# Optimization experiments

Hardware: AMD Instinct MI355X
Metric: run time of the kernel (lower is better)

## Reference

```python
import jax, jax.numpy as jnp
import numpy as np
from jax import lax

START_TAG = 29
STOP_TAG = 30
PAD_TAG = 31
NEG_INF = -10000.0


def setup_inputs() -> dict:
    key = jax.random.key(0)
    k_feat, k_trans, k_len = jax.random.split(key, 3)
    S, B, T = 1024, 1024, 32
    feats = jax.random.normal(k_feat, (S, B, T), dtype=jnp.float32)
    # left-aligned padding mask with random lengths in [S//2, S]
    lengths = jax.random.randint(k_len, (B,), S // 2, S + 1)
    mask = (jnp.arange(S)[:, None] < lengths[None, :]).astype(jnp.float32)  # [S,B]
    transitions = jax.random.normal(k_trans, (T, T), dtype=jnp.float32)
    # replicate the constraint initialization from __init__
    transitions = transitions.at[START_TAG, :].set(NEG_INF)
    transitions = transitions.at[:, STOP_TAG].set(NEG_INF)
    transitions = transitions.at[:, PAD_TAG].set(NEG_INF)
    transitions = transitions.at[PAD_TAG, :].set(NEG_INF)
    transitions = transitions.at[PAD_TAG, STOP_TAG].set(0.0)
    transitions = transitions.at[PAD_TAG, PAD_TAG].set(0.0)
    # zero emissions at padded steps, as _get_lstm_features does (feats * mask)
    feats = feats * mask[:, :, None]
    return {"feats": feats, "mask": mask, "transitions": transitions}


def reference(feats, mask, transitions):
    """CRF forward algorithm (log partition) + Viterbi max-score scan.

    feats: [S, B, T] emission scores, mask: [S, B] float, transitions: [T, T]
    (transitions[i, j] = score of transitioning from tag j to tag i).
    Returns (logZ [B], best_score [B], pointers [S, B, T] int32).
    """
    S, B, T = feats.shape

    alpha0 = jnp.full((B, T), NEG_INF, dtype=feats.dtype).at[:, START_TAG].set(0.0)

    def fwd_step(alpha, xs):
        feat, m = xs  # feat [B,T], m [B]
        # alpha_t[b, i, j] = alpha[b, j] + transitions[i, j] + feat[b, i]
        alpha_t = alpha[:, None, :] + transitions[None, :, :] + feat[:, :, None]
        new = jax.nn.logsumexp(alpha_t, axis=-1)  # [B,T]
        m = m[:, None]
        return new * m + alpha * (1.0 - m), None

    alpha, _ = lax.scan(fwd_step, alpha0, (feats, mask))
    logZ = jax.nn.logsumexp(alpha + transitions[STOP_TAG][None, :], axis=-1)  # [B]

    def vit_step(scores, xs):
        feat, m = xs
        scores_t = scores[:, None, :] + transitions[None, :, :]  # [B,T,T]
        best = jnp.max(scores_t, axis=-1)                        # [B,T]
        ptr = jnp.argmax(scores_t, axis=-1).astype(jnp.int32)    # [B,T]
        scores_t = best + feat
        m = m[:, None]
        return scores_t * m + scores * (1.0 - m), ptr

    scores0 = jnp.full((B, T), NEG_INF, dtype=feats.dtype).at[:, START_TAG].set(0.0)
    scores, pointers = lax.scan(vit_step, scores0, (feats, mask))
    scores = scores + transitions[STOP_TAG][None, :]
    best_score = jnp.max(scores, axis=-1)  # [B]
    return logZ, best_score, pointers
```

## Files before the change

### kernel.cpp

```cpp
#include <hip/hip_runtime.h>


#define SS 1024
#define BB 1024
#define TT 32
#define POFF (2 * BB)

__global__ __launch_bounds__(64) void crf_split_kernel(
    const float* __restrict__ feats,
    const float* __restrict__ mask,
    const float* __restrict__ trans,
    float* __restrict__ out) {

  const int b    = blockIdx.x;
  const int lane = threadIdx.x;
  const int g    = lane >> 5;
  const int i    = lane & 31;
  const int j0   = g << 4;

  __shared__ __align__(16) float row[TT];

  const float t_stop = trans[30 * TT + i];

  float f[4], mk[4];
#pragma unroll
  for (int u = 0; u < 4; ++u) {
    f[u]  = feats[(u * BB + b) * TT + i];
    mk[u] = mask[u * BB + b];
  }

  if (blockIdx.y == 0) {
    float er[16];
#pragma unroll
    for (int k = 0; k < 16; ++k)
      er[k] = __expf(trans[i * TT + j0 + k]);

    float alpha = (i == 29) ? 0.0f : -10000.0f;
    float M = 0.0f;

#pragma unroll 1
    for (int s = 0; s < SS; s += 4) {
      float nf[4], nm[4];
#pragma unroll
      for (int u = 0; u < 4; ++u) {
        int su = (s + 4 + u < SS) ? (s + 4 + u) : 0;
        nf[u] = feats[(su * BB + b) * TT + i];
        nm[u] = mask[su * BB + b];
      }
#pragma unroll
      for (int u = 0; u < 4; ++u) {
        if (mk[u] == 0.0f) goto fwd_done;
        float p = __expf(alpha - M);
        row[i] = p;
        __builtin_amdgcn_wave_barrier();
        float4 p0 = *(const float4*)&row[j0];
        float4 p1 = *(const float4*)&row[j0 + 4];
        float4 p2 = *(const float4*)&row[j0 + 8];
        float4 p3 = *(const float4*)&row[j0 + 12];
        __builtin_amdgcn_wave_barrier();
        float a0 = er[0] * p0.x, a1 = er[1] * p0.y;
        float a2 = er[2] * p0.z, a3 = er[3] * p0.w;
        a0 = fmaf(er[4],  p1.x, a0); a1 = fmaf(er[5],  p1.y, a1);
        a2 = fmaf(er[6],  p1.z, a2); a3 = fmaf(er[7],  p1.w, a3);
        a0 = fmaf(er[8],  p2.x, a0); a1 = fmaf(er[9],  p2.y, a1);
        a2 = fmaf(er[10], p2.z, a2); a3 = fmaf(er[11], p2.w, a3);
        a0 = fmaf(er[12], p3.x, a0); a1 = fmaf(er[13], p3.y, a1);
        a2 = fmaf(er[14], p3.z, a2); a3 = fmaf(er[15], p3.w, a3);
        float aa = (a0 + a1) + (a2 + a3);
        float D = aa + __shfl_xor(aa, 32, 64);
        alpha = M + f[u] + __logf(D);
        M = __uint_as_float(
              __builtin_amdgcn_readfirstlane(__float_as_uint(alpha)));
      }
#pragma unroll
      for (int u = 0; u < 4; ++u) { f[u] = nf[u]; mk[u] = nm[u]; }
    }
fwd_done:
    {
      float v = alpha + t_stop;
      float M2 = v;
#pragma unroll
      for (int d = 1; d < 32; d <<= 1) M2 = fmaxf(M2, __shfl_xor(M2, d, 64));
      float e = __expf(v - M2);
#pragma unroll
      for (int d = 1; d < 32; d <<= 1) e += __shfl_xor(e, d, 64);
      if (lane == 0) out[b] = M2 + __logf(e);
    }
    return;
  }

  {
    float tr[16];
#pragma unroll
    for (int k = 0; k < 16; ++k)
      tr[k] = trans[i * TT + j0 + k];

    float sc = (i == 29) ? 0.0f : -10000.0f;
    int s_exit = SS;

    auto vit_step = [&](float& best, int& ptr) {
      row[i] = sc;
      __builtin_amdgcn_wave_barrier();
      float4 s0 = *(const float4*)&row[j0];
      float4 s1 = *(const float4*)&row[j0 + 4];
      float4 s2 = *(const float4*)&row[j0 + 8];
      float4 s3 = *(const float4*)&row[j0 + 12];
      __builtin_amdgcn_wave_barrier();
      float v[16] = {s0.x, s0.y, s0.z, s0.w, s1.x, s1.y, s1.z, s1.w,
                     s2.x, s2.y, s2.z, s2.w, s3.x, s3.y, s3.z, s3.w};
      int ix[16];
#pragma unroll
      for (int k = 0; k < 16; ++k) { v[k] += tr[k]; ix[k] = j0 + k; }
#pragma unroll
      for (int st = 1; st < 16; st <<= 1) {
#pragma unroll
        for (int k = 0; k < 16; k += 2 * st) {
          bool t = v[k + st] > v[k];
          v[k]  = t ? v[k + st] : v[k];
          ix[k] = t ? ix[k + st] : ix[k];
        }
      }
      float ob = __shfl_xor(v[0], 32, 64);
      int   op = __shfl_xor(ix[0], 32, 64);
      float lowB  = g ? ob : v[0];   int lowP  = g ? op : ix[0];
      float highB = g ? v[0] : ob;   int highP = g ? ix[0] : op;
      bool t = highB > lowB;
      best = t ? highB : lowB;
      ptr  = t ? highP : lowP;
    };

#pragma unroll 1
    for (int s = 0; s < SS; s += 4) {
      float nf[4], nm[4];
#pragma unroll
      for (int u = 0; u < 4; ++u) {
        int su = (s + 4 + u < SS) ? (s + 4 + u) : 0;
        nf[u] = feats[(su * BB + b) * TT + i];
        nm[u] = mask[su * BB + b];
      }
#pragma unroll
      for (int u = 0; u < 4; ++u) {
        if (mk[u] == 0.0f) { s_exit = s + u; goto vit_tail; }
        float best; int ptr;
        vit_step(best, ptr);
        if (g == 0) out[POFF + ((s + u) * BB + b) * TT + i] = (float)ptr;
        sc = best + f[u];
      }
#pragma unroll
      for (int u = 0; u < 4; ++u) { f[u] = nf[u]; mk[u] = nm[u]; }
    }
vit_tail:
    {
      float tb; int tp;
      vit_step(tb, tp);
      float tv = (float)tp;
      for (int s2 = s_exit + g; s2 < SS; s2 += 2)
        out[POFF + (s2 * BB + b) * TT + i] = tv;

      float w = sc + t_stop;
#pragma unroll
      for (int d = 1; d < 32; d <<= 1) w = fmaxf(w, __shfl_xor(w, d, 64));
      if (lane == 0) out[BB + b] = w;
    }
  }
}

extern "C" void kernel_launch(void* const* d_in, const int* in_sizes, int n_in,
                              void* d_out, int out_size, void* d_ws, size_t ws_size,
                              hipStream_t stream) {
  const float* feats = (const float*)d_in[0];
  const float* msk   = (const float*)d_in[1];
  const float* trans = (const float*)d_in[2];
  float* out = (float*)d_out;
  (void)in_sizes; (void)n_in; (void)out_size; (void)d_ws; (void)ws_size;
  crf_split_kernel<<<dim3(BB, 2), dim3(64), 0, stream>>>(feats, msk, trans, out);
}
```

Measured before the change: 582.9 us.

## Map two batch rows per wave, one per half-wave, removing cross-half reductions

Each 64-lane wave now processes two batch elements, one per 32-lane half. Each lane does the full 32-term logsumexp dot product and the 32-way Viterbi argmax itself, so the cross-half shuffle and merge on the serial per-step chain go away. The forward rescale no longer uses a readfirstlane broadcast; it is updated from the tag-0 probability, clamped. Prefetch now looks 8 steps ahead, and early exit uses a ballot over both rows. The cost is longer per-lane dependency chains, half as many waves, and each wave looping until the longer of its two sequences ends.

```diff
diff --git a/kernel.cpp b/kernel.cpp
--- a/kernel.cpp
+++ b/kernel.cpp
@@ -6,34 +6,38 @@
 #define TT 32
 #define POFF (2 * BB)
 
-__global__ __launch_bounds__(64) void crf_split_kernel(
+__global__ __launch_bounds__(64) void crf2_kernel(
     const float* __restrict__ feats,
     const float* __restrict__ mask,
     const float* __restrict__ trans,
     float* __restrict__ out) {
 
-  const int b    = blockIdx.x;
-  const int lane = threadIdx.x;
-  const int g    = lane >> 5;
-  const int i    = lane & 31;
-  const int j0   = g << 4;
-
-  __shared__ __align__(16) float row[TT];
-
+  const int l  = threadIdx.x;
+  const int h  = l >> 5;
+  const int i  = l & 31;
+  const int b0 = blockIdx.x * 2;
+  const int b  = b0 + h;
+
+  __shared__ __align__(16) float row[64];
+
+  const float* fbase = feats + (size_t)b0 * TT + l;
+  const float* mbase = mask + b;
   const float t_stop = trans[30 * TT + i];
 
-  float f[4], mk[4];
+  float f0[4], m0[4], f1[4], m1[4];
 #pragma unroll
   for (int u = 0; u < 4; ++u) {
-    f[u]  = feats[(u * BB + b) * TT + i];
-    mk[u] = mask[u * BB + b];
+    f0[u] = fbase[(size_t)u * BB * TT];
+    m0[u] = mbase[(size_t)u * BB];
+    f1[u] = fbase[(size_t)(u + 4) * BB * TT];
+    m1[u] = mbase[(size_t)(u + 4) * BB];
   }
 
   if (blockIdx.y == 0) {
-    float er[16];
-#pragma unroll
-    for (int k = 0; k < 16; ++k)
-      er[k] = __expf(trans[i * TT + j0 + k]);
+    float er[32];
+#pragma unroll
+    for (int k = 0; k < 32; ++k)
+      er[k] = __expf(trans[i * TT + k]);
 
     float alpha = (i == 29) ? 0.0f : -10000.0f;
     float M = 0.0f;
@@ -43,37 +47,46 @@
       float nf[4], nm[4];
 #pragma unroll
       for (int u = 0; u < 4; ++u) {
-        int su = (s + 4 + u < SS) ? (s + 4 + u) : 0;
-        nf[u] = feats[(su * BB + b) * TT + i];
-        nm[u] = mask[su * BB + b];
-      }
-#pragma unroll
-      for (int u = 0; u < 4; ++u) {
-        if (mk[u] == 0.0f) goto fwd_done;
+        int su = (s + 8 + u < SS) ? (s + 8 + u) : 0;
+        nf[u] = fbase[(size_t)su * BB * TT];
+        nm[u] = mbase[(size_t)su * BB];
+      }
+#pragma unroll
+      for (int u = 0; u < 4; ++u) {
+        bool act = (m0[u] != 0.0f);
+        if (__ballot(act) == 0ull) goto fwd_done;
         float p = __expf(alpha - M);
-        row[i] = p;
+        row[l] = p;
         __builtin_amdgcn_wave_barrier();
-        float4 p0 = *(const float4*)&row[j0];
-        float4 p1 = *(const float4*)&row[j0 + 4];
-        float4 p2 = *(const float4*)&row[j0 + 8];
-        float4 p3 = *(const float4*)&row[j0 + 12];
+        const float4* q = (const float4*)&row[h * 32];
+        float4 q0 = q[0], q1 = q[1], q2 = q[2], q3 = q[3];
+        float4 q4 = q[4], q5 = q[5], q6 = q[6], q7 = q[7];
         __builtin_amdgcn_wave_barrier();
-        float a0 = er[0] * p0.x, a1 = er[1] * p0.y;
-        float a2 = er[2] * p0.z, a3 = er[3] * p0.w;
-        a0 = fmaf(er[4],  p1.x, a0); a1 = fmaf(er[5],  p1.y, a1);
-        a2 = fmaf(er[6],  p1.z, a2); a3 = fmaf(er[7],  p1.w, a3);
-        a0 = fmaf(er[8],  p2.x, a0); a1 = fmaf(er[9],  p2.y, a1);
-        a2 = fmaf(er[10], p2.z, a2); a3 = fmaf(er[11], p2.w, a3);
-        a0 = fmaf(er[12], p3.x, a0); a1 = fmaf(er[13], p3.y, a1);
-        a2 = fmaf(er[14], p3.z, a2); a3 = fmaf(er[15], p3.w, a3);
-        float aa = (a0 + a1) + (a2 + a3);
-        float D = aa + __shfl_xor(aa, 32, 64);
-        alpha = M + f[u] + __logf(D);
-        M = __uint_as_float(
-              __builtin_amdgcn_readfirstlane(__float_as_uint(alpha)));
-      }
-#pragma unroll
-      for (int u = 0; u < 4; ++u) { f[u] = nf[u]; mk[u] = nm[u]; }
+        float a0 = er[0] * q0.x, a1 = er[1] * q0.y;
+        float a2 = er[2] * q0.z, a3 = er[3] * q0.w;
+        a0 = fmaf(er[4],  q1.x, a0); a1 = fmaf(er[5],  q1.y, a1);
+        a2 = fmaf(er[6],  q1.z, a2); a3 = fmaf(er[7],  q1.w, a3);
+        a0 = fmaf(er[8],  q2.x, a0); a1 = fmaf(er[9],  q2.y, a1);
+        a2 = fmaf(er[10], q2.z, a2); a3 = fmaf(er[11], q2.w, a3);
+        a0 = fmaf(er[12], q3.x, a0); a1 = fmaf(er[13], q3.y, a1);
+        a2 = fmaf(er[14], q3.z, a2); a3 = fmaf(er[15], q3.w, a3);
+        a0 = fmaf(er[16], q4.x, a0); a1 = fmaf(er[17], q4.y, a1);
+        a2 = fmaf(er[18], q4.z, a2); a3 = fmaf(er[19], q4.w, a3);
+        a0 = fmaf(er[20], q5.x, a0); a1 = fmaf(er[21], q5.y, a1);
+        a2 = fmaf(er[22], q5.z, a2); a3 = fmaf(er[23], q5.w, a3);
+        a0 = fmaf(er[24], q6.x, a0); a1 = fmaf(er[25], q6.y, a1);
+        a2 = fmaf(er[26], q6.z, a2); a3 = fmaf(er[27], q6.w, a3);
+        a0 = fmaf(er[28], q7.x, a0); a1 = fmaf(er[29], q7.y, a1);
+        a2 = fmaf(er[30], q7.z, a2); a3 = fmaf(er[31], q7.w, a3);
+        float D = (a0 + a1) + (a2 + a3);
+        float nv = M + f0[u] + __logf(D);
+        alpha = act ? nv : alpha;
+        M = M + fmaxf(__logf(q0.x), -20.0f);
+      }
+#pragma unroll
+      for (int u = 0; u < 4; ++u) {
+        f0[u] = f1[u]; m0[u] = m1[u]; f1[u] = nf[u]; m1[u] = nm[u];
+      }
     }
 fwd_done:
     {
@@ -84,49 +97,57 @@
       float e = __expf(v - M2);
 #pragma unroll
       for (int d = 1; d < 32; d <<= 1) e += __shfl_xor(e, d, 64);
-      if (lane == 0) out[b] = M2 + __logf(e);
+      if (i == 0) out[b] = M2 + __logf(e);
     }
     return;
   }
 
   {
-    float tr[16];
-#pragma unroll
-    for (int k = 0; k < 16; ++k)
-      tr[k] = trans[i * TT + j0 + k];
+    float tr[32];
+#pragma unroll
+    for (int k = 0; k < 32; ++k) tr[k] = trans[i * TT + k];
 
     float sc = (i == 29) ? 0.0f : -10000.0f;
     int s_exit = SS;
 
-    auto vit_step = [&](float& best, int& ptr) {
-      row[i] = sc;
+    auto vstep = [&](float& best, int& ptr) {
+      row[l] = sc;
       __builtin_amdgcn_wave_barrier();
-      float4 s0 = *(const float4*)&row[j0];
-      float4 s1 = *(const float4*)&row[j0 + 4];
-      float4 s2 = *(const float4*)&row[j0 + 8];
-      float4 s3 = *(const float4*)&row[j0 + 12];
+      const float4* q = (const float4*)&row[h * 32];
+      float4 q0 = q[0], q1 = q[1], q2 = q[2], q3 = q[3];
+      float4 q4 = q[4], q5 = q[5], q6 = q[6], q7 = q[7];
       __builtin_amdgcn_wave_barrier();
-      float v[16] = {s0.x, s0.y, s0.z, s0.w, s1.x, s1.y, s1.z, s1.w,
-                     s2.x, s2.y, s2.z, s2.w, s3.x, s3.y, s3.z, s3.w};
-      int ix[16];
-#pragma unroll
-      for (int k = 0; k < 16; ++k) { v[k] += tr[k]; ix[k] = j0 + k; }
-#pragma unroll
-      for (int st = 1; st < 16; st <<= 1) {
-#pragma unroll
-        for (int k = 0; k < 16; k += 2 * st) {
+      float v[32];
+      v[0]  = q0.x + tr[0];  v[1]  = q0.y + tr[1];
+      v[2]  = q0.z + tr[2];  v[3]  = q0.w + tr[3];
+      v[4]  = q1.x + tr[4];  v[5]  = q1.y + tr[5];
+      v[6]  = q1.z + tr[6];  v[7]  = q1.w + tr[7];
+      v[8]  = q2.x + tr[8];  v[9]  = q2.y + tr[9];
+      v[10] = q2.z + tr[10]; v[11] = q2.w + tr[11];
+      v[12] = q3.x + tr[12]; v[13] = q3.y + tr[13];
+      v[14] = q3.z + tr[14]; v[15] = q3.w + tr[15];
+      v[16] = q4.x + tr[16]; v[17] = q4.y + tr[17];
+      v[18] = q4.z + tr[18]; v[19] = q4.w + tr[19];
+      v[20] = q5.x + tr[20]; v[21] = q5.y + tr[21];
+      v[22] = q5.z + tr[22]; v[23] = q5.w + tr[23];
+      v[24] = q6.x + tr[24]; v[25] = q6.y + tr[25];
+      v[26] = q6.z + tr[26]; v[27] = q6.w + tr[27];
+      v[28] = q7.x + tr[28]; v[29] = q7.y + tr[29];
+      v[30] = q7.z + tr[30]; v[31] = q7.w + tr[31];
+      int ix[32];
+#pragma unroll
+      for (int k = 0; k < 32; ++k) ix[k] = k;
+#pragma unroll
+      for (int st = 1; st < 32; st <<= 1) {
+#pragma unroll
+        for (int k = 0; k < 32; k += 2 * st) {
           bool t = v[k + st] > v[k];
           v[k]  = t ? v[k + st] : v[k];
           ix[k] = t ? ix[k + st] : ix[k];
         }
       }
-      float ob = __shfl_xor(v[0], 32, 64);
-      int   op = __shfl_xor(ix[0], 32, 64);
-      float lowB  = g ? ob : v[0];   int lowP  = g ? op : ix[0];
-      float highB = g ? v[0] : ob;   int highP = g ? ix[0] : op;
-      bool t = highB > lowB;
-      best = t ? highB : lowB;
-      ptr  = t ? highP : lowP;
+      best = v[0];
+      ptr  = ix[0];
     };
 
 #pragma unroll 1
@@ -134,33 +155,36 @@
       float nf[4], nm[4];
 #pragma unroll
       for (int u = 0; u < 4; ++u) {
-        int su = (s + 4 + u < SS) ? (s + 4 + u) : 0;
-        nf[u] = feats[(su * BB + b) * TT + i];
-        nm[u] = mask[su * BB + b];
-      }
-#pragma unroll
-      for (int u = 0; u < 4; ++u) {
-        if (mk[u] == 0.0f) { s_exit = s + u; goto vit_tail; }
+        int su = (s + 8 + u < SS) ? (s + 8 + u) : 0;
+        nf[u] = fbase[(size_t)su * BB * TT];
+        nm[u] = mbase[(size_t)su * BB];
+      }
+#pragma unroll
+      for (int u = 0; u < 4; ++u) {
+        bool act = (m0[u] != 0.0f);
+        if (__ballot(act) == 0ull) { s_exit = s + u; goto vit_tail; }
         float best; int ptr;
-        vit_step(best, ptr);
-        if (g == 0) out[POFF + ((s + u) * BB + b) * TT + i] = (float)ptr;
-        sc = best + f[u];
-      }
-#pragma unroll
-      for (int u = 0; u < 4; ++u) { f[u] = nf[u]; mk[u] = nm[u]; }
+        vstep(best, ptr);
+        out[POFF + (size_t)(s + u) * BB * TT + b0 * TT + l] = (float)ptr;
+        sc = act ? best + f0[u] : sc;
+      }
+#pragma unroll
+      for (int u = 0; u < 4; ++u) {
+        f0[u] = f1[u]; m0[u] = m1[u]; f1[u] = nf[u]; m1[u] = nm[u];
+      }
     }
 vit_tail:
     {
       float tb; int tp;
-      vit_step(tb, tp);
-      float tv = (float)tp;
-      for (int s2 = s_exit + g; s2 < SS; s2 += 2)
-        out[POFF + (s2 * BB + b) * TT + i] = tv;
+      vstep(tb, tp);
+      float tj = (float)tp;
+      for (int s2 = s_exit; s2 < SS; ++s2)
+        out[POFF + (size_t)s2 * BB * TT + b0 * TT + l] = tj;
 
       float w = sc + t_stop;
 #pragma unroll
       for (int d = 1; d < 32; d <<= 1) w = fmaxf(w, __shfl_xor(w, d, 64));
-      if (lane == 0) out[BB + b] = w;
+      if (i == 0) out[BB + b] = w;
     }
   }
 }
@@ -173,5 +197,5 @@
   const float* trans = (const float*)d_in[2];
   float* out = (float*)d_out;
   (void)in_sizes; (void)n_in; (void)out_size; (void)d_ws; (void)ws_size;
-  crf_split_kernel<<<dim3(BB, 2), dim3(64), 0, stream>>>(feats, msk, trans, out);
+  crf2_kernel<<<dim3(BB / 2, 2), dim3(64), 0, stream>>>(feats, msk, trans, out);
 }
```

New measurement: 577.2 us. No clear change (-1.0%).
